# Kernel optimization log

Measured on AMD Instinct MI355X. Metric: run time of the kernel, lower is better.

## Reference

```python
import jax, jax.numpy as jnp
import numpy as np

N = 100_000   # nodes per type
E = 800_000   # edges per relation
H = 128       # hidden_channels
O = 64        # out_channels
TIME_SCALE = 1.0
LN_EPS = 1e-5


def setup_inputs() -> dict:
    key = jax.random.key(0)
    ks = jax.random.split(key, 24)
    nrm = lambda k, shp, s=1.0: jax.random.normal(k, shp, jnp.float32) * s
    inp = {}
    inp["x_A"] = nrm(ks[0], (N, H))
    inp["x_B"] = nrm(ks[1], (N, H))
    inp["x_C"] = nrm(ks[2], (N, H))
    inp["t_A"] = jax.random.uniform(ks[3], (N,), jnp.float32) * 1000.0
    inp["t_B"] = jax.random.uniform(ks[4], (N,), jnp.float32) * 1000.0
    inp["t_C"] = jax.random.uniform(ks[5], (N,), jnp.float32) * 1000.0
    inp["edge1"] = jnp.stack([jax.random.randint(ks[6], (E,), 0, N),
                              jax.random.randint(ks[7], (E,), 0, N)]).astype(jnp.int32)
    inp["edge2"] = jnp.stack([jax.random.randint(ks[8], (E,), 0, N),
                              jax.random.randint(ks[9], (E,), 0, N)]).astype(jnp.int32)
    kk = 10
    for i in range(2):
        inp[f"Wl{i}"] = nrm(ks[kk], (H, H), 0.05); kk += 1
        inp[f"bl{i}"] = jnp.zeros((H,), jnp.float32)
        inp[f"W0{i}"] = nrm(ks[kk], (H, H), 0.05); kk += 1
        inp[f"b0{i}"] = jnp.zeros((H,), jnp.float32)
        inp[f"W1{i}"] = nrm(ks[kk], (H, H), 0.05); kk += 1
        inp[f"b1{i}"] = jnp.zeros((H,), jnp.float32)
        inp[f"gate{i}"] = jnp.asarray(0.5, jnp.float32)
        inp[f"lam{i}"] = jnp.asarray(0.1, jnp.float32)  # raw lambda
        inp[f"lng{i}"] = jnp.ones((H,), jnp.float32)
        inp[f"lnb{i}"] = jnp.zeros((H,), jnp.float32)
    inp["Wout"] = nrm(ks[kk], (H, O), 0.05)
    inp["bout"] = jnp.zeros((O,), jnp.float32)
    return inp


def _layer(h_src, h_dst, x0_dst, edge, t_src, t_dst,
           Wl, bl, W0, b0, W1, b1, gate, raw_lam, lng, lnb):
    s, d = edge[0], edge[1]
    n_dst = h_dst.shape[0]
    # per-edge time-decay weight
    lam = jax.nn.softplus(raw_lam) + 1e-8
    delta = jnp.maximum((t_dst[d] - t_src[s]) / TIME_SCALE, 0.0)
    w = jnp.exp(jnp.maximum(-lam * delta, -60.0))          # [E]
    # gather + weight + scatter-add  (propagate with aggr='add')
    msg = h_src[s] * w[:, None]                            # [E,H]
    agg = jax.ops.segment_sum(msg, d, num_segments=n_dst)  # [n_dst,H]
    deg = jnp.maximum(jax.ops.segment_sum(w, d, num_segments=n_dst), 1e-6)
    out = agg / deg[:, None]
    g = jax.nn.sigmoid(gate)
    y = out @ Wl + bl + (1.0 - g) * (h_dst @ W0 + b0) + g * (x0_dst @ W1 + b1)
    y = jax.nn.relu(y)
    mu = jnp.mean(y, axis=-1, keepdims=True)
    var = jnp.mean((y - mu) ** 2, axis=-1, keepdims=True)
    y = (y - mu) * jax.lax.rsqrt(var + LN_EPS) * lng + lnb
    # index_copy_: only nodes that appear as a destination get updated
    cnt = jax.ops.segment_sum(jnp.ones_like(w), d, num_segments=n_dst)
    return jnp.where((cnt > 0)[:, None], y, h_dst)


def reference(x_A, x_B, x_C, t_A, t_B, t_C, edge1, edge2,
              Wl0, bl0, W00, b00, W10, b10, gate0, lam0, lng0, lnb0,
              Wl1, bl1, W01, b01, W11, b11, gate1, lam1, lng1, lnb1,
              Wout, bout):
    # reversed(metapath): process (B,r2,C) with conv_idx=1 first, then (A,r1,B) with conv_idx=0
    h_C = _layer(x_B, x_C, x_C, edge2, t_B, t_C,
                 Wl1, bl1, W01, b01, W11, b11, gate1, lam1, lng1, lnb1)
    h_B = _layer(x_A, x_B, x_B, edge1, t_A, t_B,
                 Wl0, bl0, W00, b00, W10, b10, gate0, lam0, lng0, lnb0)
    del h_B  # target type is metapath[-1][2] == 'C'; B's update does not feed C
    return h_C @ Wout + bout
```

## Files before the change

kernel.cpp:

```cpp
#include <hip/hip_runtime.h>


#define HD 128
#define OD 64
#define SCAN_E 1024

typedef unsigned short u16;
typedef short v8s __attribute__((ext_vector_type(8)));
typedef float v4f __attribute__((ext_vector_type(4)));

union Frag {
    unsigned int u[4];
    uint4 q;
    v8s v;
};

__device__ __forceinline__ float softplus_f(float x) {
    return fmaxf(x, 0.0f) + log1pf(expf(-fabsf(x)));
}
__device__ __forceinline__ float sigmoid_f(float x) {
    return 1.0f / (1.0f + expf(-x));
}
__device__ __forceinline__ int swz(int r, int c) {
    int g = (c >> 2) ^ (r & 7);
    return r * 128 + g * 4 + (c & 3);
}

__device__ __forceinline__ void split_store(float x, u16* ph, u16* pl) {
    unsigned int b = __float_as_uint(x);
    unsigned int h = b & 0xffff0000u;
    *ph = (u16)(h >> 16);
    float r = x - __uint_as_float(h);
    *pl = (u16)(__float_as_uint(r) >> 16);
}

__device__ __forceinline__ void cvt_split8(const float* f, unsigned int* hi,
                                           unsigned int* lo) {
#pragma unroll
    for (int j = 0; j < 4; ++j) {
        unsigned int b0 = __float_as_uint(f[2 * j]);
        unsigned int b1 = __float_as_uint(f[2 * j + 1]);
        unsigned int h0 = b0 & 0xffff0000u;
        unsigned int h1 = b1 & 0xffff0000u;
        hi[j] = (h0 >> 16) | h1;
        float r0 = f[2 * j]     - __uint_as_float(h0);
        float r1 = f[2 * j + 1] - __uint_as_float(h1);
        lo[j] = (__float_as_uint(r0) >> 16) | (__float_as_uint(r1) & 0xffff0000u);
    }
}

__global__ __launch_bounds__(256) void k_prep(
    const int* __restrict__ edge, int* __restrict__ cnt, int E, int gE,
    const float* __restrict__ Wl, const float* __restrict__ W0,
    const float* __restrict__ W1, const float* __restrict__ Wout,
    const float* __restrict__ bl, const float* __restrict__ b0,
    const float* __restrict__ b1, const float* __restrict__ gatep,
    u16* __restrict__ wlh, u16* __restrict__ wll,
    u16* __restrict__ wch, u16* __restrict__ wcl,
    u16* __restrict__ woh, u16* __restrict__ wol, float* __restrict__ bc)
{
    if (blockIdx.x < (unsigned)gE) {
        int e = blockIdx.x * 256 + threadIdx.x;
        if (e < E) atomicAdd(cnt + edge[E + e], 1);
        return;
    }
    int i = (blockIdx.x - gE) * 256 + threadIdx.x;
    const float g = sigmoid_f(gatep[0]);
    if (i < 16384) {
        int n = i >> 7, k = i & 127;
        float a  = Wl[k * 128 + n];
        float w0 = W0[k * 128 + n];
        float w1 = W1[k * 128 + n];
        float c  = (1.f - g) * w0 + g * w1;
        int off = (((k >> 5) * 8 + (n >> 4)) * 64 +
                   ((k & 31) >> 3) * 16 + (n & 15)) * 8 + (k & 7);
        split_store(a, wlh + off, wll + off);
        split_store(c, wch + off, wcl + off);
    } else if (i < 24576) {
        int j = i - 16384;
        int n = j >> 7, k = j & 127;
        float v = Wout[k * 64 + n];
        int off = (((k >> 5) * 4 + (n >> 4)) * 64 +
                   ((k & 31) >> 3) * 16 + (n & 15)) * 8 + (k & 7);
        split_store(v, woh + off, wol + off);
    } else if (i < 24704) {
        int t = i - 24576;
        bc[t] = bl[t] + (1.f - g) * b0[t] + g * b1[t];
    }
}

__global__ __launch_bounds__(256) void k_scan1(
    const int* __restrict__ cnt, int* __restrict__ offs,
    int* __restrict__ part, int* __restrict__ tot, int N)
{
    __shared__ int sh[256];
    const int t = threadIdx.x;
    const int base = blockIdx.x * SCAN_E + t * 4;
    int v[4], sum = 0;
#pragma unroll
    for (int i = 0; i < 4; ++i) {
        int idx = base + i;
        v[i] = (idx < N) ? cnt[idx] : 0;
        sum += v[i];
    }
    sh[t] = sum;
    __syncthreads();
    for (int off = 1; off < 256; off <<= 1) {
        int x = (t >= off) ? sh[t - off] : 0;
        __syncthreads();
        sh[t] += x;
        __syncthreads();
    }
    int run = (t > 0) ? sh[t - 1] : 0;
    if (t == 255) part[blockIdx.x] = atomicAdd(tot, sh[255]);
#pragma unroll
    for (int i = 0; i < 4; ++i) {
        int idx = base + i;
        if (idx < N) offs[idx] = run;
        run += v[i];
    }
}

__global__ __launch_bounds__(256) void k_fillw(
    const int* __restrict__ edge, const float* __restrict__ tB,
    const float* __restrict__ tC, const float* __restrict__ lam_raw,
    const int* __restrict__ offs, const int* __restrict__ part,
    int* __restrict__ fillc, int2* __restrict__ srcw, int E)
{
    int e = blockIdx.x * 256 + threadIdx.x;
    if (e >= E) return;
    int s = edge[e];
    int d = edge[E + e];
    float lam = softplus_f(lam_raw[0]) + 1e-8f;
    float dt  = fmaxf(tC[d] - tB[s], 0.0f);
    float w   = expf(fmaxf(-lam * dt, -60.0f));
    int pos = offs[d] + part[d >> 10] + atomicAdd(fillc + d, 1);
    srcw[pos] = make_int2(s, __float_as_int(w));
}

__global__ __launch_bounds__(256) void k_gather(
    const float* __restrict__ xB, const int2* __restrict__ srcw,
    const int* __restrict__ offs, const int* __restrict__ part,
    const int* __restrict__ cnt, float* __restrict__ aggn, int N)
{
    const int wave = (blockIdx.x * 256 + threadIdx.x) >> 6;
    const int lane = threadIdx.x & 63;
    const int slot = lane >> 4;
    const int l4   = lane & 15;
    if (wave >= N) return;
    const int r    = wave;
    const int degc = cnt[r];

    float* dstp = aggn + (size_t)r * HD;
    if (degc == 0) {
        if (slot == 0) {
            *reinterpret_cast<float4*>(dstp + l4 * 4) = make_float4(0, 0, 0, 0);
            *reinterpret_cast<float4*>(dstp + 64 + l4 * 4) = make_float4(0, 0, 0, 0);
        }
        return;
    }

    const int start = offs[r] + part[r >> 10];
    float4 a0 = make_float4(0, 0, 0, 0), a1 = make_float4(0, 0, 0, 0);
    float sw = 0.f;
#pragma unroll 2
    for (int j = slot; j < degc; j += 4) {
        int2 swp = srcw[start + j];
        float w = __int_as_float(swp.y);
        const float* row = xB + (size_t)swp.x * HD;
        float4 x0 = *reinterpret_cast<const float4*>(row + l4 * 4);
        float4 x1 = *reinterpret_cast<const float4*>(row + 64 + l4 * 4);
        a0.x = fmaf(w, x0.x, a0.x); a0.y = fmaf(w, x0.y, a0.y);
        a0.z = fmaf(w, x0.z, a0.z); a0.w = fmaf(w, x0.w, a0.w);
        a1.x = fmaf(w, x1.x, a1.x); a1.y = fmaf(w, x1.y, a1.y);
        a1.z = fmaf(w, x1.z, a1.z); a1.w = fmaf(w, x1.w, a1.w);
        sw += w;
    }
#pragma unroll
    for (int m = 16; m <= 32; m <<= 1) {
        a0.x += __shfl_xor(a0.x, m); a0.y += __shfl_xor(a0.y, m);
        a0.z += __shfl_xor(a0.z, m); a0.w += __shfl_xor(a0.w, m);
        a1.x += __shfl_xor(a1.x, m); a1.y += __shfl_xor(a1.y, m);
        a1.z += __shfl_xor(a1.z, m); a1.w += __shfl_xor(a1.w, m);
        sw   += __shfl_xor(sw, m);
    }
    float inv = 1.0f / fmaxf(sw, 1e-6f);
    if (slot == 0) {
        a0.x *= inv; a0.y *= inv; a0.z *= inv; a0.w *= inv;
        a1.x *= inv; a1.y *= inv; a1.z *= inv; a1.w *= inv;
        *reinterpret_cast<float4*>(dstp + l4 * 4) = a0;
        *reinterpret_cast<float4*>(dstp + 64 + l4 * 4) = a1;
    }
}

__global__ __launch_bounds__(256) void k_fused(
    const float* __restrict__ xC, const float* __restrict__ aggn,
    const int* __restrict__ cnt,
    const u16* __restrict__ wlh, const u16* __restrict__ wll,
    const u16* __restrict__ wch, const u16* __restrict__ wcl,
    const u16* __restrict__ woh, const u16* __restrict__ wol,
    const float* __restrict__ bc, const float* __restrict__ lng,
    const float* __restrict__ lnb, const float* __restrict__ bout,
    float* __restrict__ out, int N)
{
    __shared__ float lds[4 * 32 * 128];

    const int lane = threadIdx.x & 63;
    const int wid  = threadIdx.x >> 6;
    const int lr   = lane & 15;
    const int kb   = lane >> 4;
    const int row0 = blockIdx.x * 128 + wid * 32;
    float* myl = lds + wid * 32 * 128;

    v4f acc[2][8] = {};

#pragma unroll
    for (int mat = 0; mat < 2; ++mat) {
        const float* Asrc = mat ? xC : aggn;
        const uint4* BH = (const uint4*)(mat ? wch : wlh);
        const uint4* BL = (const uint4*)(mat ? wcl : wll);
#pragma unroll
        for (int kc = 0; kc < 4; ++kc) {
            Frag ah[2], al[2];
#pragma unroll
            for (int rt = 0; rt < 2; ++rt) {
                int r = row0 + rt * 16 + lr;
                r = (r < N) ? r : (N - 1);
                const float4* ap = (const float4*)(
                    Asrc + (size_t)r * HD + kc * 32 + kb * 8);
                float4 u0 = ap[0], u1 = ap[1];
                float f[8] = {u0.x, u0.y, u0.z, u0.w, u1.x, u1.y, u1.z, u1.w};
                cvt_split8(f, ah[rt].u, al[rt].u);
            }
#pragma unroll
            for (int ct = 0; ct < 8; ++ct) {
                int idx = (kc * 8 + ct) * 64 + lane;
                Frag bh, bl;
                bh.q = BH[idx];
                bl.q = BL[idx];
#pragma unroll
                for (int rt = 0; rt < 2; ++rt) {
                    acc[rt][ct] = __builtin_amdgcn_mfma_f32_16x16x32_bf16(
                        ah[rt].v, bh.v, acc[rt][ct], 0, 0, 0);
                    acc[rt][ct] = __builtin_amdgcn_mfma_f32_16x16x32_bf16(
                        ah[rt].v, bl.v, acc[rt][ct], 0, 0, 0);
                    acc[rt][ct] = __builtin_amdgcn_mfma_f32_16x16x32_bf16(
                        al[rt].v, bh.v, acc[rt][ct], 0, 0, 0);
                }
            }
        }
    }

    float bcv[8], gav[8], bev[8];
#pragma unroll
    for (int ct = 0; ct < 8; ++ct) {
        int c = ct * 16 + lr;
        bcv[ct] = bc[c];
        gav[ct] = lng[c];
        bev[ct] = lnb[c];
    }

#pragma unroll
    for (int rt = 0; rt < 2; ++rt) {
        int rq = row0 + rt * 16 + kb * 4;
        int cvr[4] = {0, 0, 0, 0};
        if (rq < N) {
            int4 cv = *(const int4*)(cnt + rq);
            cvr[0] = cv.x; cvr[1] = cv.y; cvr[2] = cv.z; cvr[3] = cv.w;
        }
#pragma unroll
        for (int reg = 0; reg < 4; ++reg) {
            int rloc = rt * 16 + kb * 4 + reg;
            int r    = rq + reg;
            float yv[8];
            float s = 0.f, q = 0.f;
#pragma unroll
            for (int ct = 0; ct < 8; ++ct) {
                float v = acc[rt][ct][reg] + bcv[ct];
                v = fmaxf(v, 0.0f);
                yv[ct] = v;
                s += v;
                q += v * v;
            }
#pragma unroll
            for (int m = 1; m < 16; m <<= 1) {
                s += __shfl_xor(s, m);
                q += __shfl_xor(q, m);
            }
            float mu   = s * (1.0f / 128.0f);
            float var  = q * (1.0f / 128.0f) - mu * mu;
            float rstd = rsqrtf(var + 1e-5f);

            if (r < N) {
                if (cvr[reg] > 0) {
#pragma unroll
                    for (int ct = 0; ct < 8; ++ct)
                        myl[swz(rloc, ct * 16 + lr)] =
                            (yv[ct] - mu) * rstd * gav[ct] + bev[ct];
                } else {
                    size_t base = (size_t)r * HD;
#pragma unroll
                    for (int ct = 0; ct < 8; ++ct)
                        myl[swz(rloc, ct * 16 + lr)] = xC[base + ct * 16 + lr];
                }
            } else {
#pragma unroll
                for (int ct = 0; ct < 8; ++ct)
                    myl[swz(rloc, ct * 16 + lr)] = 0.0f;
            }
        }
    }

    __syncthreads();

    v4f acc2[2][4] = {};
    const uint4* BH3 = (const uint4*)woh;
    const uint4* BL3 = (const uint4*)wol;

#pragma unroll
    for (int kc = 0; kc < 4; ++kc) {
        Frag ah[2], al[2];
#pragma unroll
        for (int rt = 0; rt < 2; ++rt) {
            int rloc = rt * 16 + lr;
            int c0   = kc * 32 + kb * 8;
            float4 u0 = *reinterpret_cast<const float4*>(&myl[swz(rloc, c0)]);
            float4 u1 = *reinterpret_cast<const float4*>(&myl[swz(rloc, c0 + 4)]);
            float f[8] = {u0.x, u0.y, u0.z, u0.w, u1.x, u1.y, u1.z, u1.w};
            cvt_split8(f, ah[rt].u, al[rt].u);
        }
#pragma unroll
        for (int ct = 0; ct < 4; ++ct) {
            int idx = (kc * 4 + ct) * 64 + lane;
            Frag bh, bl;
            bh.q = BH3[idx];
            bl.q = BL3[idx];
#pragma unroll
            for (int rt = 0; rt < 2; ++rt) {
                acc2[rt][ct] = __builtin_amdgcn_mfma_f32_16x16x32_bf16(
                    ah[rt].v, bh.v, acc2[rt][ct], 0, 0, 0);
                acc2[rt][ct] = __builtin_amdgcn_mfma_f32_16x16x32_bf16(
                    ah[rt].v, bl.v, acc2[rt][ct], 0, 0, 0);
                acc2[rt][ct] = __builtin_amdgcn_mfma_f32_16x16x32_bf16(
                    al[rt].v, bh.v, acc2[rt][ct], 0, 0, 0);
            }
        }
    }

    float bov[4];
#pragma unroll
    for (int ct = 0; ct < 4; ++ct) bov[ct] = bout[ct * 16 + lr];

#pragma unroll
    for (int rt = 0; rt < 2; ++rt) {
#pragma unroll
        for (int reg = 0; reg < 4; ++reg) {
            int r = row0 + rt * 16 + kb * 4 + reg;
            if (r < N) {
#pragma unroll
                for (int ct = 0; ct < 4; ++ct)
                    out[(size_t)r * OD + ct * 16 + lr] =
                        acc2[rt][ct][reg] + bov[ct];
            }
        }
    }
}

extern "C" void kernel_launch(void* const* d_in, const int* in_sizes, int n_in,
                              void* d_out, int out_size, void* d_ws, size_t ws_size,
                              hipStream_t stream) {
    const float* xB    = (const float*)d_in[1];
    const float* xC    = (const float*)d_in[2];
    const float* tB    = (const float*)d_in[4];
    const float* tC    = (const float*)d_in[5];
    const int*   edge2 = (const int*)d_in[7];
    const float* Wl1   = (const float*)d_in[18];
    const float* bl1   = (const float*)d_in[19];
    const float* W01   = (const float*)d_in[20];
    const float* b01   = (const float*)d_in[21];
    const float* W11   = (const float*)d_in[22];
    const float* b11   = (const float*)d_in[23];
    const float* gate1 = (const float*)d_in[24];
    const float* lam1  = (const float*)d_in[25];
    const float* lng1  = (const float*)d_in[26];
    const float* lnb1  = (const float*)d_in[27];
    const float* Wout  = (const float*)d_in[28];
    const float* bout  = (const float*)d_in[29];

    const int N = in_sizes[2] / HD;
    const int E = in_sizes[7] / 2;

    int*   cnt   = (int*)d_ws;
    int*   fillc = cnt + N;
    int*   offs  = fillc + N;
    int*   part  = offs + N;
    int*   tot   = part + 128;
    int2*  srcw  = (int2*)(tot + 4);
    u16*   wlh   = (u16*)(srcw + E);
    u16*   wll   = wlh + 16384;
    u16*   wch   = wll + 16384;
    u16*   wcl   = wch + 16384;
    u16*   woh   = wcl + 16384;
    u16*   wol   = woh + 8192;
    float* bc    = (float*)(wol + 8192);
    float* buf   = bc + 128;

    hipMemsetAsync(cnt, 0, (size_t)2 * N * sizeof(int), stream);
    hipMemsetAsync(tot, 0, sizeof(int), stream);

    dim3 blk(256);
    const int gE = (E + 255) / 256;
    const int NB = (N + SCAN_E - 1) / SCAN_E;

    k_prep <<<gE + 97, blk, 0, stream>>>(edge2, cnt, E, gE,
                                         Wl1, W01, W11, Wout, bl1, b01, b11,
                                         gate1, wlh, wll, wch, wcl, woh, wol, bc);
    k_scan1<<<NB, blk, 0, stream>>>(cnt, offs, part, tot, N);
    k_fillw<<<gE, blk, 0, stream>>>(edge2, tB, tC, lam1, offs, part, fillc, srcw, E);

    const int gN64 = (N * 64 + 255) / 256;
    k_gather<<<gN64, blk, 0, stream>>>(xB, srcw, offs, part, cnt, buf, N);

    const int GB = (N + 127) / 128;
    k_fused<<<GB, blk, 0, stream>>>(xC, buf, cnt, wlh, wll, wch, wcl, woh, wol,
                                    bc, lng1, lnb1, bout, (float*)d_out, N);
}
```

Baseline: 219.2 us.

## Widen gather edge parallelism and retile fused GEMM to 64 rows per wave

The gather kernel now splits each destination row across 8 edge slots of 8 lanes each, with every lane loading four float4 chunks, instead of 4 slots of 16 lanes. The aim is more edges in flight per wave to hide gather latency. The fused kernel now uses 128-thread blocks in which each wave handles 64 rows, so each loaded weight fragment is reused over four row tiles. The output GEMM now runs per 16-row tile straight from a small per-wave LDS buffer, with no block barrier. The larger accumulator arrays raise register pressure and may reduce occupancy.

```diff
diff --git a/kernel.cpp b/kernel.cpp
--- a/kernel.cpp
+++ b/kernel.cpp
@@ -145,55 +145,63 @@
 {
     const int wave = (blockIdx.x * 256 + threadIdx.x) >> 6;
     const int lane = threadIdx.x & 63;
-    const int slot = lane >> 4;
-    const int l4   = lane & 15;
+    const int slot = lane >> 3;
+    const int l3   = lane & 7;
     if (wave >= N) return;
     const int r    = wave;
     const int degc = cnt[r];
 
-    float* dstp = aggn + (size_t)r * HD;
+    float* dstp = aggn + (size_t)r * HD + l3 * 16;
     if (degc == 0) {
         if (slot == 0) {
-            *reinterpret_cast<float4*>(dstp + l4 * 4) = make_float4(0, 0, 0, 0);
-            *reinterpret_cast<float4*>(dstp + 64 + l4 * 4) = make_float4(0, 0, 0, 0);
+            float4 z = make_float4(0, 0, 0, 0);
+#pragma unroll
+            for (int c = 0; c < 4; ++c)
+                *reinterpret_cast<float4*>(dstp + c * 4) = z;
         }
         return;
     }
 
     const int start = offs[r] + part[r >> 10];
-    float4 a0 = make_float4(0, 0, 0, 0), a1 = make_float4(0, 0, 0, 0);
+    float4 a[4] = {make_float4(0, 0, 0, 0), make_float4(0, 0, 0, 0),
+                   make_float4(0, 0, 0, 0), make_float4(0, 0, 0, 0)};
     float sw = 0.f;
-#pragma unroll 2
-    for (int j = slot; j < degc; j += 4) {
+    for (int j = slot; j < degc; j += 8) {
         int2 swp = srcw[start + j];
         float w = __int_as_float(swp.y);
-        const float* row = xB + (size_t)swp.x * HD;
-        float4 x0 = *reinterpret_cast<const float4*>(row + l4 * 4);
-        float4 x1 = *reinterpret_cast<const float4*>(row + 64 + l4 * 4);
-        a0.x = fmaf(w, x0.x, a0.x); a0.y = fmaf(w, x0.y, a0.y);
-        a0.z = fmaf(w, x0.z, a0.z); a0.w = fmaf(w, x0.w, a0.w);
-        a1.x = fmaf(w, x1.x, a1.x); a1.y = fmaf(w, x1.y, a1.y);
-        a1.z = fmaf(w, x1.z, a1.z); a1.w = fmaf(w, x1.w, a1.w);
+        const float* row = xB + (size_t)swp.x * HD + l3 * 16;
+#pragma unroll
+        for (int c = 0; c < 4; ++c) {
+            float4 x = *reinterpret_cast<const float4*>(row + c * 4);
+            a[c].x = fmaf(w, x.x, a[c].x);
+            a[c].y = fmaf(w, x.y, a[c].y);
+            a[c].z = fmaf(w, x.z, a[c].z);
+            a[c].w = fmaf(w, x.w, a[c].w);
+        }
         sw += w;
     }
 #pragma unroll
-    for (int m = 16; m <= 32; m <<= 1) {
-        a0.x += __shfl_xor(a0.x, m); a0.y += __shfl_xor(a0.y, m);
-        a0.z += __shfl_xor(a0.z, m); a0.w += __shfl_xor(a0.w, m);
-        a1.x += __shfl_xor(a1.x, m); a1.y += __shfl_xor(a1.y, m);
-        a1.z += __shfl_xor(a1.z, m); a1.w += __shfl_xor(a1.w, m);
-        sw   += __shfl_xor(sw, m);
+    for (int m = 8; m <= 32; m <<= 1) {
+#pragma unroll
+        for (int c = 0; c < 4; ++c) {
+            a[c].x += __shfl_xor(a[c].x, m);
+            a[c].y += __shfl_xor(a[c].y, m);
+            a[c].z += __shfl_xor(a[c].z, m);
+            a[c].w += __shfl_xor(a[c].w, m);
+        }
+        sw += __shfl_xor(sw, m);
     }
     float inv = 1.0f / fmaxf(sw, 1e-6f);
     if (slot == 0) {
-        a0.x *= inv; a0.y *= inv; a0.z *= inv; a0.w *= inv;
-        a1.x *= inv; a1.y *= inv; a1.z *= inv; a1.w *= inv;
-        *reinterpret_cast<float4*>(dstp + l4 * 4) = a0;
-        *reinterpret_cast<float4*>(dstp + 64 + l4 * 4) = a1;
-    }
-}
-
-__global__ __launch_bounds__(256) void k_fused(
+#pragma unroll
+        for (int c = 0; c < 4; ++c) {
+            a[c].x *= inv; a[c].y *= inv; a[c].z *= inv; a[c].w *= inv;
+            *reinterpret_cast<float4*>(dstp + c * 4) = a[c];
+        }
+    }
+}
+
+__global__ __launch_bounds__(128) void k_fused(
     const float* __restrict__ xC, const float* __restrict__ aggn,
     const int* __restrict__ cnt,
     const u16* __restrict__ wlh, const u16* __restrict__ wll,
@@ -203,16 +211,16 @@
     const float* __restrict__ lnb, const float* __restrict__ bout,
     float* __restrict__ out, int N)
 {
-    __shared__ float lds[4 * 32 * 128];
+    __shared__ float lds[2 * 16 * 128];
 
     const int lane = threadIdx.x & 63;
     const int wid  = threadIdx.x >> 6;
     const int lr   = lane & 15;
     const int kb   = lane >> 4;
-    const int row0 = blockIdx.x * 128 + wid * 32;
-    float* myl = lds + wid * 32 * 128;
-
-    v4f acc[2][8] = {};
+    const int row0 = blockIdx.x * 128 + wid * 64;
+    float* myl = lds + wid * 16 * 128;
+
+    v4f acc[4][8] = {};
 
 #pragma unroll
     for (int mat = 0; mat < 2; ++mat) {
@@ -221,9 +229,9 @@
         const uint4* BL = (const uint4*)(mat ? wcl : wll);
 #pragma unroll
         for (int kc = 0; kc < 4; ++kc) {
-            Frag ah[2], al[2];
-#pragma unroll
-            for (int rt = 0; rt < 2; ++rt) {
+            Frag ah[4], al[4];
+#pragma unroll
+            for (int rt = 0; rt < 4; ++rt) {
                 int r = row0 + rt * 16 + lr;
                 r = (r < N) ? r : (N - 1);
                 const float4* ap = (const float4*)(
@@ -239,7 +247,7 @@
                 bh.q = BH[idx];
                 bl.q = BL[idx];
 #pragma unroll
-                for (int rt = 0; rt < 2; ++rt) {
+                for (int rt = 0; rt < 4; ++rt) {
                     acc[rt][ct] = __builtin_amdgcn_mfma_f32_16x16x32_bf16(
                         ah[rt].v, bh.v, acc[rt][ct], 0, 0, 0);
                     acc[rt][ct] = __builtin_amdgcn_mfma_f32_16x16x32_bf16(
@@ -259,9 +267,15 @@
         gav[ct] = lng[c];
         bev[ct] = lnb[c];
     }
-
-#pragma unroll
-    for (int rt = 0; rt < 2; ++rt) {
+    float bov[4];
+#pragma unroll
+    for (int ct = 0; ct < 4; ++ct) bov[ct] = bout[ct * 16 + lr];
+
+    const uint4* BH3 = (const uint4*)woh;
+    const uint4* BL3 = (const uint4*)wol;
+
+#pragma unroll
+    for (int rt = 0; rt < 4; ++rt) {
         int rq = row0 + rt * 16 + kb * 4;
         int cvr[4] = {0, 0, 0, 0};
         if (rq < N) {
@@ -270,7 +284,7 @@
         }
 #pragma unroll
         for (int reg = 0; reg < 4; ++reg) {
-            int rloc = rt * 16 + kb * 4 + reg;
+            int rloc = kb * 4 + reg;
             int r    = rq + reg;
             float yv[8];
             float s = 0.f, q = 0.f;
@@ -309,58 +323,40 @@
                     myl[swz(rloc, ct * 16 + lr)] = 0.0f;
             }
         }
-    }
-
-    __syncthreads();
-
-    v4f acc2[2][4] = {};
-    const uint4* BH3 = (const uint4*)woh;
-    const uint4* BL3 = (const uint4*)wol;
-
-#pragma unroll
-    for (int kc = 0; kc < 4; ++kc) {
-        Frag ah[2], al[2];
-#pragma unroll
-        for (int rt = 0; rt < 2; ++rt) {
-            int rloc = rt * 16 + lr;
-            int c0   = kc * 32 + kb * 8;
-            float4 u0 = *reinterpret_cast<const float4*>(&myl[swz(rloc, c0)]);
-            float4 u1 = *reinterpret_cast<const float4*>(&myl[swz(rloc, c0 + 4)]);
-            float f[8] = {u0.x, u0.y, u0.z, u0.w, u1.x, u1.y, u1.z, u1.w};
-            cvt_split8(f, ah[rt].u, al[rt].u);
-        }
-#pragma unroll
-        for (int ct = 0; ct < 4; ++ct) {
-            int idx = (kc * 4 + ct) * 64 + lane;
-            Frag bh, bl;
-            bh.q = BH3[idx];
-            bl.q = BL3[idx];
-#pragma unroll
-            for (int rt = 0; rt < 2; ++rt) {
-                acc2[rt][ct] = __builtin_amdgcn_mfma_f32_16x16x32_bf16(
-                    ah[rt].v, bh.v, acc2[rt][ct], 0, 0, 0);
-                acc2[rt][ct] = __builtin_amdgcn_mfma_f32_16x16x32_bf16(
-                    ah[rt].v, bl.v, acc2[rt][ct], 0, 0, 0);
-                acc2[rt][ct] = __builtin_amdgcn_mfma_f32_16x16x32_bf16(
-                    al[rt].v, bh.v, acc2[rt][ct], 0, 0, 0);
-            }
-        }
-    }
-
-    float bov[4];
-#pragma unroll
-    for (int ct = 0; ct < 4; ++ct) bov[ct] = bout[ct * 16 + lr];
-
-#pragma unroll
-    for (int rt = 0; rt < 2; ++rt) {
+
+        v4f acc2[4] = {};
+#pragma unroll
+        for (int kc = 0; kc < 4; ++kc) {
+            Frag ah, al;
+            {
+                int c0 = kc * 32 + kb * 8;
+                float4 u0 = *reinterpret_cast<const float4*>(&myl[swz(lr, c0)]);
+                float4 u1 = *reinterpret_cast<const float4*>(&myl[swz(lr, c0 + 4)]);
+                float f[8] = {u0.x, u0.y, u0.z, u0.w, u1.x, u1.y, u1.z, u1.w};
+                cvt_split8(f, ah.u, al.u);
+            }
+#pragma unroll
+            for (int ct = 0; ct < 4; ++ct) {
+                int idx = (kc * 4 + ct) * 64 + lane;
+                Frag bh, bl;
+                bh.q = BH3[idx];
+                bl.q = BL3[idx];
+                acc2[ct] = __builtin_amdgcn_mfma_f32_16x16x32_bf16(
+                    ah.v, bh.v, acc2[ct], 0, 0, 0);
+                acc2[ct] = __builtin_amdgcn_mfma_f32_16x16x32_bf16(
+                    ah.v, bl.v, acc2[ct], 0, 0, 0);
+                acc2[ct] = __builtin_amdgcn_mfma_f32_16x16x32_bf16(
+                    al.v, bh.v, acc2[ct], 0, 0, 0);
+            }
+        }
+
 #pragma unroll
         for (int reg = 0; reg < 4; ++reg) {
-            int r = row0 + rt * 16 + kb * 4 + reg;
+            int r = rq + reg;
             if (r < N) {
 #pragma unroll
                 for (int ct = 0; ct < 4; ++ct)
-                    out[(size_t)r * OD + ct * 16 + lr] =
-                        acc2[rt][ct][reg] + bov[ct];
+                    out[(size_t)r * OD + ct * 16 + lr] = acc2[ct][reg] + bov[ct];
             }
         }
     }
@@ -422,6 +418,7 @@
     k_gather<<<gN64, blk, 0, stream>>>(xB, srcw, offs, part, cnt, buf, N);
 
     const int GB = (N + 127) / 128;
-    k_fused<<<GB, blk, 0, stream>>>(xC, buf, cnt, wlh, wll, wch, wcl, woh, wol,
-                                    bc, lng1, lnb1, bout, (float*)d_out, N);
-}
+    k_fused<<<GB, dim3(128), 0, stream>>>(xC, buf, cnt,
+                                          wlh, wll, wch, wcl, woh, wol,
+                                          bc, lng1, lnb1, bout, (float*)d_out, N);
+}
```

After: 246.7 us. +12.5%, slower.

## Interleave output GEMM per row tile to halve LDS and double block size

Applied to the files above, without the earlier changes.

The fused kernel now does the output projection right after each 16-row tile is normalized, instead of staging all 32 rows per wave. This halves the per-wave LDS staging area and drops the block-wide barrier, since each wave reads only its own LDS region. Blocks grow to 512 threads covering 256 rows, and the second-stage accumulators shrink from 8 to 4 vectors. The aim is to lower LDS and register use and raise occupancy. The cost is that the Wout fragments are reloaded once per row tile.

```diff
diff --git a/kernel.cpp b/kernel.cpp
--- a/kernel.cpp
+++ b/kernel.cpp
@@ -193,7 +193,7 @@
     }
 }
 
-__global__ __launch_bounds__(256) void k_fused(
+__global__ __launch_bounds__(512) void k_fused(
     const float* __restrict__ xC, const float* __restrict__ aggn,
     const int* __restrict__ cnt,
     const u16* __restrict__ wlh, const u16* __restrict__ wll,
@@ -203,14 +203,14 @@
     const float* __restrict__ lnb, const float* __restrict__ bout,
     float* __restrict__ out, int N)
 {
-    __shared__ float lds[4 * 32 * 128];
+    __shared__ float lds[8 * 16 * 128];
 
     const int lane = threadIdx.x & 63;
     const int wid  = threadIdx.x >> 6;
     const int lr   = lane & 15;
     const int kb   = lane >> 4;
-    const int row0 = blockIdx.x * 128 + wid * 32;
-    float* myl = lds + wid * 32 * 128;
+    const int row0 = blockIdx.x * 256 + wid * 32;
+    float* myl = lds + wid * 16 * 128;
 
     v4f acc[2][8] = {};
 
@@ -259,6 +259,12 @@
         gav[ct] = lng[c];
         bev[ct] = lnb[c];
     }
+    float bov[4];
+#pragma unroll
+    for (int ct = 0; ct < 4; ++ct) bov[ct] = bout[ct * 16 + lr];
+
+    const uint4* BH3 = (const uint4*)woh;
+    const uint4* BL3 = (const uint4*)wol;
 
 #pragma unroll
     for (int rt = 0; rt < 2; ++rt) {
@@ -270,7 +276,7 @@
         }
 #pragma unroll
         for (int reg = 0; reg < 4; ++reg) {
-            int rloc = rt * 16 + kb * 4 + reg;
+            int rloc = kb * 4 + reg;
             int r    = rq + reg;
             float yv[8];
             float s = 0.f, q = 0.f;
@@ -309,58 +315,40 @@
                     myl[swz(rloc, ct * 16 + lr)] = 0.0f;
             }
         }
-    }
-
-    __syncthreads();
-
-    v4f acc2[2][4] = {};
-    const uint4* BH3 = (const uint4*)woh;
-    const uint4* BL3 = (const uint4*)wol;
-
-#pragma unroll
-    for (int kc = 0; kc < 4; ++kc) {
-        Frag ah[2], al[2];
-#pragma unroll
-        for (int rt = 0; rt < 2; ++rt) {
-            int rloc = rt * 16 + lr;
-            int c0   = kc * 32 + kb * 8;
-            float4 u0 = *reinterpret_cast<const float4*>(&myl[swz(rloc, c0)]);
-            float4 u1 = *reinterpret_cast<const float4*>(&myl[swz(rloc, c0 + 4)]);
-            float f[8] = {u0.x, u0.y, u0.z, u0.w, u1.x, u1.y, u1.z, u1.w};
-            cvt_split8(f, ah[rt].u, al[rt].u);
-        }
-#pragma unroll
-        for (int ct = 0; ct < 4; ++ct) {
-            int idx = (kc * 4 + ct) * 64 + lane;
-            Frag bh, bl;
-            bh.q = BH3[idx];
-            bl.q = BL3[idx];
-#pragma unroll
-            for (int rt = 0; rt < 2; ++rt) {
-                acc2[rt][ct] = __builtin_amdgcn_mfma_f32_16x16x32_bf16(
-                    ah[rt].v, bh.v, acc2[rt][ct], 0, 0, 0);
-                acc2[rt][ct] = __builtin_amdgcn_mfma_f32_16x16x32_bf16(
-                    ah[rt].v, bl.v, acc2[rt][ct], 0, 0, 0);
-                acc2[rt][ct] = __builtin_amdgcn_mfma_f32_16x16x32_bf16(
-                    al[rt].v, bh.v, acc2[rt][ct], 0, 0, 0);
-            }
-        }
-    }
-
-    float bov[4];
-#pragma unroll
-    for (int ct = 0; ct < 4; ++ct) bov[ct] = bout[ct * 16 + lr];
-
-#pragma unroll
-    for (int rt = 0; rt < 2; ++rt) {
+
+        v4f acc2[4] = {};
+#pragma unroll
+        for (int kc = 0; kc < 4; ++kc) {
+            Frag ah, al;
+            {
+                int c0 = kc * 32 + kb * 8;
+                float4 u0 = *reinterpret_cast<const float4*>(&myl[swz(lr, c0)]);
+                float4 u1 = *reinterpret_cast<const float4*>(&myl[swz(lr, c0 + 4)]);
+                float f[8] = {u0.x, u0.y, u0.z, u0.w, u1.x, u1.y, u1.z, u1.w};
+                cvt_split8(f, ah.u, al.u);
+            }
+#pragma unroll
+            for (int ct = 0; ct < 4; ++ct) {
+                int idx = (kc * 4 + ct) * 64 + lane;
+                Frag bh, bl;
+                bh.q = BH3[idx];
+                bl.q = BL3[idx];
+                acc2[ct] = __builtin_amdgcn_mfma_f32_16x16x32_bf16(
+                    ah.v, bh.v, acc2[ct], 0, 0, 0);
+                acc2[ct] = __builtin_amdgcn_mfma_f32_16x16x32_bf16(
+                    ah.v, bl.v, acc2[ct], 0, 0, 0);
+                acc2[ct] = __builtin_amdgcn_mfma_f32_16x16x32_bf16(
+                    al.v, bh.v, acc2[ct], 0, 0, 0);
+            }
+        }
+
 #pragma unroll
         for (int reg = 0; reg < 4; ++reg) {
-            int r = row0 + rt * 16 + kb * 4 + reg;
+            int r = rq + reg;
             if (r < N) {
 #pragma unroll
                 for (int ct = 0; ct < 4; ++ct)
-                    out[(size_t)r * OD + ct * 16 + lr] =
-                        acc2[rt][ct][reg] + bov[ct];
+                    out[(size_t)r * OD + ct * 16 + lr] = acc2[ct][reg] + bov[ct];
             }
         }
     }
@@ -421,7 +409,8 @@
     const int gN64 = (N * 64 + 255) / 256;
     k_gather<<<gN64, blk, 0, stream>>>(xB, srcw, offs, part, cnt, buf, N);
 
-    const int GB = (N + 127) / 128;
-    k_fused<<<GB, blk, 0, stream>>>(xC, buf, cnt, wlh, wll, wch, wcl, woh, wol,
-                                    bc, lng1, lnb1, bout, (float*)d_out, N);
-}
+    const int GB = (N + 255) / 256;
+    k_fused<<<GB, dim3(512), 0, stream>>>(xC, buf, cnt,
+                                          wlh, wll, wch, wcl, woh, wol,
+                                          bc, lng1, lnb1, bout, (float*)d_out, N);
+}
```

New measurement: 226.6 us. 1.03x slower.

## Overlap xC@Wcombined GEMM with gather by merging into one launch

Applied to the files above, without the earlier changes.

Moves the x0/h_dst matmul (xC times combined W0/W1 weights) out of the fused epilogue kernel into a new kernel that also performs the edge gather, with separate block ranges doing each task. This lets the compute-bound MFMA work run alongside the memory-bound gather. In exchange it writes a full N×128 fp32 partial result to global memory and reads it back in the epilogue, which adds about 100 MB of traffic.

```diff
diff --git a/kernel.cpp b/kernel.cpp
--- a/kernel.cpp
+++ b/kernel.cpp
@@ -138,12 +138,71 @@
     srcw[pos] = make_int2(s, __float_as_int(w));
 }
 
-__global__ __launch_bounds__(256) void k_gather(
-    const float* __restrict__ xB, const int2* __restrict__ srcw,
-    const int* __restrict__ offs, const int* __restrict__ part,
-    const int* __restrict__ cnt, float* __restrict__ aggn, int N)
+__global__ __launch_bounds__(256) void k_mix(
+    const float* __restrict__ xB, const float* __restrict__ xC,
+    const int2* __restrict__ srcw, const int* __restrict__ offs,
+    const int* __restrict__ part, const int* __restrict__ cnt,
+    const u16* __restrict__ wch, const u16* __restrict__ wcl,
+    float* __restrict__ aggn, float* __restrict__ accg, int GBx, int N)
 {
-    const int wave = (blockIdx.x * 256 + threadIdx.x) >> 6;
+    if (blockIdx.x < (unsigned)GBx) {
+        const int lane = threadIdx.x & 63;
+        const int wid  = threadIdx.x >> 6;
+        const int lr   = lane & 15;
+        const int kb   = lane >> 4;
+        const int row0 = blockIdx.x * 128 + wid * 32;
+
+        v4f acc[2][8] = {};
+        const uint4* BH = (const uint4*)wch;
+        const uint4* BL = (const uint4*)wcl;
+
+#pragma unroll
+        for (int kc = 0; kc < 4; ++kc) {
+            Frag ah[2], al[2];
+#pragma unroll
+            for (int rt = 0; rt < 2; ++rt) {
+                int r = row0 + rt * 16 + lr;
+                r = (r < N) ? r : (N - 1);
+                const float4* ap = (const float4*)(
+                    xC + (size_t)r * HD + kc * 32 + kb * 8);
+                float4 u0 = ap[0], u1 = ap[1];
+                float f[8] = {u0.x, u0.y, u0.z, u0.w, u1.x, u1.y, u1.z, u1.w};
+                cvt_split8(f, ah[rt].u, al[rt].u);
+            }
+#pragma unroll
+            for (int ct = 0; ct < 8; ++ct) {
+                int idx = (kc * 8 + ct) * 64 + lane;
+                Frag bh, bl;
+                bh.q = BH[idx];
+                bl.q = BL[idx];
+#pragma unroll
+                for (int rt = 0; rt < 2; ++rt) {
+                    acc[rt][ct] = __builtin_amdgcn_mfma_f32_16x16x32_bf16(
+                        ah[rt].v, bh.v, acc[rt][ct], 0, 0, 0);
+                    acc[rt][ct] = __builtin_amdgcn_mfma_f32_16x16x32_bf16(
+                        ah[rt].v, bl.v, acc[rt][ct], 0, 0, 0);
+                    acc[rt][ct] = __builtin_amdgcn_mfma_f32_16x16x32_bf16(
+                        al[rt].v, bh.v, acc[rt][ct], 0, 0, 0);
+                }
+            }
+        }
+#pragma unroll
+        for (int rt = 0; rt < 2; ++rt) {
+            int rq = row0 + rt * 16 + kb * 4;
+#pragma unroll
+            for (int reg = 0; reg < 4; ++reg) {
+                int r = rq + reg;
+                if (r < N) {
+#pragma unroll
+                    for (int ct = 0; ct < 8; ++ct)
+                        accg[(size_t)r * HD + ct * 16 + lr] = acc[rt][ct][reg];
+                }
+            }
+        }
+        return;
+    }
+
+    const int wave = ((blockIdx.x - GBx) * 256 + threadIdx.x) >> 6;
     const int lane = threadIdx.x & 63;
     const int slot = lane >> 4;
     const int l4   = lane & 15;
@@ -195,9 +254,8 @@
 
 __global__ __launch_bounds__(256) void k_fused(
     const float* __restrict__ xC, const float* __restrict__ aggn,
-    const int* __restrict__ cnt,
+    const float* __restrict__ accg, const int* __restrict__ cnt,
     const u16* __restrict__ wlh, const u16* __restrict__ wll,
-    const u16* __restrict__ wch, const u16* __restrict__ wcl,
     const u16* __restrict__ woh, const u16* __restrict__ wol,
     const float* __restrict__ bc, const float* __restrict__ lng,
     const float* __restrict__ lnb, const float* __restrict__ bout,
@@ -213,12 +271,9 @@
     float* myl = lds + wid * 32 * 128;
 
     v4f acc[2][8] = {};
-
-#pragma unroll
-    for (int mat = 0; mat < 2; ++mat) {
-        const float* Asrc = mat ? xC : aggn;
-        const uint4* BH = (const uint4*)(mat ? wch : wlh);
-        const uint4* BL = (const uint4*)(mat ? wcl : wll);
+    {
+        const uint4* BH = (const uint4*)wlh;
+        const uint4* BL = (const uint4*)wll;
 #pragma unroll
         for (int kc = 0; kc < 4; ++kc) {
             Frag ah[2], al[2];
@@ -227,7 +282,7 @@
                 int r = row0 + rt * 16 + lr;
                 r = (r < N) ? r : (N - 1);
                 const float4* ap = (const float4*)(
-                    Asrc + (size_t)r * HD + kc * 32 + kb * 8);
+                    aggn + (size_t)r * HD + kc * 32 + kb * 8);
                 float4 u0 = ap[0], u1 = ap[1];
                 float f[8] = {u0.x, u0.y, u0.z, u0.w, u1.x, u1.y, u1.z, u1.w};
                 cvt_split8(f, ah[rt].u, al[rt].u);
@@ -274,13 +329,19 @@
             int r    = rq + reg;
             float yv[8];
             float s = 0.f, q = 0.f;
-#pragma unroll
-            for (int ct = 0; ct < 8; ++ct) {
-                float v = acc[rt][ct][reg] + bcv[ct];
-                v = fmaxf(v, 0.0f);
-                yv[ct] = v;
-                s += v;
-                q += v * v;
+            if (r < N) {
+#pragma unroll
+                for (int ct = 0; ct < 8; ++ct) {
+                    float v = acc[rt][ct][reg] + bcv[ct] +
+                              accg[(size_t)r * HD + ct * 16 + lr];
+                    v = fmaxf(v, 0.0f);
+                    yv[ct] = v;
+                    s += v;
+                    q += v * v;
+                }
+            } else {
+#pragma unroll
+                for (int ct = 0; ct < 8; ++ct) yv[ct] = 0.0f;
             }
 #pragma unroll
             for (int m = 1; m < 16; m <<= 1) {
@@ -404,6 +465,7 @@
     u16*   wol   = woh + 8192;
     float* bc    = (float*)(wol + 8192);
     float* buf   = bc + 128;
+    float* accg  = buf + (size_t)N * HD;
 
     hipMemsetAsync(cnt, 0, (size_t)2 * N * sizeof(int), stream);
     hipMemsetAsync(tot, 0, sizeof(int), stream);
@@ -418,10 +480,11 @@
     k_scan1<<<NB, blk, 0, stream>>>(cnt, offs, part, tot, N);
     k_fillw<<<gE, blk, 0, stream>>>(edge2, tB, tC, lam1, offs, part, fillc, srcw, E);
 
+    const int GBx  = (N + 127) / 128;
     const int gN64 = (N * 64 + 255) / 256;
-    k_gather<<<gN64, blk, 0, stream>>>(xB, srcw, offs, part, cnt, buf, N);
-
-    const int GB = (N + 127) / 128;
-    k_fused<<<GB, blk, 0, stream>>>(xC, buf, cnt, wlh, wll, wch, wcl, woh, wol,
-                                    bc, lng1, lnb1, bout, (float*)d_out, N);
-}
+    k_mix<<<GBx + gN64, blk, 0, stream>>>(xB, xC, srcw, offs, part, cnt,
+                                          wch, wcl, buf, accg, GBx, N);
+
+    k_fused<<<GBx, blk, 0, stream>>>(xC, buf, accg, cnt, wlh, wll, woh, wol,
+                                     bc, lng1, lnb1, bout, (float*)d_out, N);
+}
```

New measurement: 257.2 us. 1.17x slower.
